# Kernel optimization log

Hardware: AMD Instinct MI355X
Metric: run time of the kernel (lower is better)

Reference implementation:

```python
import jax, jax.numpy as jnp
from jax import lax
import numpy as np

N = 8192
N_ITERS = 10  # ipf(W, 10, 1, 1): row target = 1, col target = 1


def setup_inputs() -> dict:
    key = jax.random.key(0)
    W = jax.random.normal(key, (N, N), dtype=jnp.float32)
    return {"W": W}


def reference(W):
    def step(M, _):
        # row-sum normalize to target 1, then col-sum normalize to target 1
        M = M / jnp.sum(M, axis=1, keepdims=True)
        M = M / jnp.sum(M, axis=0, keepdims=True)
        return M, None

    M = jnp.abs(W)
    M, _ = lax.scan(step, M, None, length=N_ITERS)
    return M
```

## Files before the change

kernel.cpp:

```cpp
#include <hip/hip_runtime.h>

#define N 8192

__device__ __forceinline__ unsigned int f2bf_rne(float f) {
    unsigned int u = __float_as_uint(f);
    u += 0x7fffu + ((u >> 16) & 1u);
    return u >> 16;
}
__device__ __forceinline__ unsigned int pack2(float a, float b) {
    return f2bf_rne(a) | (f2bf_rne(b) << 16);
}
__device__ __forceinline__ float bf_lo(unsigned int u) { return __uint_as_float(u << 16); }
__device__ __forceinline__ float bf_hi(unsigned int u) { return __uint_as_float(u & 0xffff0000u); }

__global__ __launch_bounds__(256) void prep(const float* __restrict__ W,
                                            unsigned int* __restrict__ A,
                                            float* __restrict__ R,
                                            float* __restrict__ b0) {
    const int tid = threadIdx.x;
    if (blockIdx.x < 32) b0[blockIdx.x * 256 + tid] = 0.0f;

    const int wave = tid >> 6, lane = tid & 63;
    const int row = blockIdx.x * 4 + wave;
    const float4* wr = (const float4*)(W + (size_t)row * N);
    uint4* ar = (uint4*)(A + (size_t)row * (N / 2));
    float s = 0.0f;
#pragma unroll 4
    for (int it = 0; it < 16; it++) {
        int g = it * 64 + lane;
        float4 w0 = wr[2 * g];
        float4 w1 = wr[2 * g + 1];
        uint4 p;
        p.x = pack2(fabsf(w0.x), fabsf(w0.y));
        p.y = pack2(fabsf(w0.z), fabsf(w0.w));
        p.z = pack2(fabsf(w1.x), fabsf(w1.y));
        p.w = pack2(fabsf(w1.z), fabsf(w1.w));
        ar[g] = p;
        s += ((bf_lo(p.x) + bf_hi(p.x)) + (bf_lo(p.y) + bf_hi(p.y))) +
             ((bf_lo(p.z) + bf_hi(p.z)) + (bf_lo(p.w) + bf_hi(p.w)));
    }
    for (int off = 32; off > 0; off >>= 1) s += __shfl_down(s, off);
    if (lane == 0) R[row] = 1.0f / s;
}

__global__ __launch_bounds__(256) void pass_rows(const unsigned short* __restrict__ A,
                                                 const float* __restrict__ b_prev,
                                                 float* __restrict__ R,
                                                 float* __restrict__ b_next) {
    __shared__ float crcp[N];
    const int tid = threadIdx.x;
#pragma unroll
    for (int k = 0; k < 8; k++) {
        int f = k * 256 + tid;
        float4 b = ((const float4*)b_prev)[f];
        float4 c;
        c.x = 1.0f / b.x; c.y = 1.0f / b.y; c.z = 1.0f / b.z; c.w = 1.0f / b.w;
        ((float4*)crcp)[f] = c;
    }
    if (tid < 8) b_next[blockIdx.x * 8 + tid] = 0.0f;
    __syncthreads();

    const int wave = tid >> 6, lane = tid & 63;
    for (int rr = 0; rr < 2; rr++) {
        const int row = blockIdx.x * 8 + wave * 2 + rr;
        const uint2* ar = (const uint2*)(A + (size_t)row * N);
        float4 a0 = {0, 0, 0, 0}, a1 = {0, 0, 0, 0};
#pragma unroll 8
        for (int k = 0; k < 32; k += 2) {
            int f0 = k * 64 + lane;
            int f1 = f0 + 64;
            uint2 u0 = ar[f0];
            uint2 u1 = ar[f1];
            float4 c0 = ((const float4*)crcp)[f0];
            float4 c1 = ((const float4*)crcp)[f1];
            a0.x = fmaf(bf_lo(u0.x), c0.x, a0.x);
            a0.y = fmaf(bf_hi(u0.x), c0.y, a0.y);
            a0.z = fmaf(bf_lo(u0.y), c0.z, a0.z);
            a0.w = fmaf(bf_hi(u0.y), c0.w, a0.w);
            a1.x = fmaf(bf_lo(u1.x), c1.x, a1.x);
            a1.y = fmaf(bf_hi(u1.x), c1.y, a1.y);
            a1.z = fmaf(bf_lo(u1.y), c1.z, a1.z);
            a1.w = fmaf(bf_hi(u1.y), c1.w, a1.w);
        }
        float s = ((a0.x + a1.x) + (a0.y + a1.y)) + ((a0.z + a1.z) + (a0.w + a1.w));
        for (int off = 32; off > 0; off >>= 1) s += __shfl_down(s, off);
        if (lane == 0) R[row] = 1.0f / s;
    }
}

__global__ __launch_bounds__(256) void pass_cols(const unsigned short* __restrict__ A,
                                                 const float* __restrict__ R,
                                                 float* __restrict__ b_next) {
    __shared__ float rloc[128];
    const int tid = threadIdx.x;
    const int ctile = blockIdx.x & 7;
    const int chunk = blockIdx.x >> 3;
    const int row0 = chunk * 128;

    if (tid < 128) rloc[tid] = R[row0 + tid];
    __syncthreads();

    const int f = ctile * 256 + tid;
    const uint2* Af = (const uint2*)A;
    float4 acc = {0, 0, 0, 0};
#pragma unroll 4
    for (int i = 0; i < 128; i++) {
        uint2 u = Af[(size_t)(row0 + i) * (N / 4) + f];
        float r = rloc[i];
        acc.x = fmaf(bf_lo(u.x), r, acc.x);
        acc.y = fmaf(bf_hi(u.x), r, acc.y);
        acc.z = fmaf(bf_lo(u.y), r, acc.z);
        acc.w = fmaf(bf_hi(u.y), r, acc.w);
    }
    float* dst = b_next + f * 4;
    atomicAdd(dst + 0, acc.x);
    atomicAdd(dst + 1, acc.y);
    atomicAdd(dst + 2, acc.z);
    atomicAdd(dst + 3, acc.w);
}

__global__ __launch_bounds__(256) void finalize(const float* __restrict__ W,
                                                const float* __restrict__ R,
                                                const float* __restrict__ b_last,
                                                float* __restrict__ out) {
    __shared__ float crcp[N];
    const int tid = threadIdx.x;
#pragma unroll
    for (int k = 0; k < 8; k++) {
        int f = k * 256 + tid;
        float4 b = ((const float4*)b_last)[f];
        float4 c;
        c.x = 1.0f / b.x; c.y = 1.0f / b.y; c.z = 1.0f / b.z; c.w = 1.0f / b.w;
        ((float4*)crcp)[f] = c;
    }
    __syncthreads();

    const int wave = tid >> 6, lane = tid & 63;
    const int row0 = blockIdx.x * 8 + wave * 2;
    for (int rr = 0; rr < 2; rr++) {
        const int row = row0 + rr;
        const float r = R[row];
        const float4* wr = (const float4*)(W + (size_t)row * N);
        float4* orow = (float4*)(out + (size_t)row * N);
#pragma unroll 4
        for (int k = 0; k < 32; k++) {
            int f = k * 64 + lane;
            float4 w = wr[f];
            float4 c = ((const float4*)crcp)[f];
            float4 o;
            o.x = r * fabsf(w.x) * c.x;
            o.y = r * fabsf(w.y) * c.y;
            o.z = r * fabsf(w.z) * c.z;
            o.w = r * fabsf(w.w) * c.w;
            orow[f] = o;
        }
    }
}

extern "C" void kernel_launch(void* const* d_in, const int* in_sizes, int n_in,
                              void* d_out, int out_size, void* d_ws, size_t ws_size,
                              hipStream_t stream) {
    const float* W = (const float*)d_in[0];
    float* out = (float*)d_out;

    unsigned short* A = (unsigned short*)d_out;

    float* R  = (float*)d_ws;
    float* b0 = R + N;
    float* b1 = b0 + N;

    prep<<<2048, 256, 0, stream>>>(W, (unsigned int*)A, R, b0);
    pass_cols<<<512, 256, 0, stream>>>(A, R, b0);

    float* bprev = b0;
    float* bnext = b1;
    for (int k = 2; k <= 10; k++) {
        pass_rows<<<1024, 256, 0, stream>>>(A, bprev, R, bnext);
        pass_cols<<<512, 256, 0, stream>>>(A, R, bnext);
        float* t = bprev; bprev = bnext; bnext = t;
    }
    finalize<<<1024, 256, 0, stream>>>(W, R, bprev, out);
}
```

Measured before the change: 956.2 us.

## Fuse row and column passes into one register-resident pass with partial column sums

Each block loads two rows per wave of the bf16 matrix into registers once, computes the row sums against cached column reciprocals, then accumulates the row-scaled values into shared-memory column sums. It writes per-block partials that a separate kernel reduces and inverts. This removes the second full read of the matrix per iteration and the global atomics. In exchange it adds a partial-sum buffer write/read, LDS atomics and high register pressure.

```diff
diff --git a/kernel.cpp b/kernel.cpp
--- a/kernel.cpp
+++ b/kernel.cpp
@@ -1,6 +1,9 @@
 #include <hip/hip_runtime.h>
 
 #define N 8192
+#define GBLK 512
+#define RPB 16
+#define TPB 512
 
 __device__ __forceinline__ unsigned int f2bf_rne(float f) {
     unsigned int u = __float_as_uint(f);
@@ -15,11 +18,8 @@
 
 __global__ __launch_bounds__(256) void prep(const float* __restrict__ W,
                                             unsigned int* __restrict__ A,
-                                            float* __restrict__ R,
-                                            float* __restrict__ b0) {
-    const int tid = threadIdx.x;
-    if (blockIdx.x < 32) b0[blockIdx.x * 256 + tid] = 0.0f;
-
+                                            float* __restrict__ R) {
+    const int tid = threadIdx.x;
     const int wave = tid >> 6, lane = tid & 63;
     const int row = blockIdx.x * 4 + wave;
     const float4* wr = (const float4*)(W + (size_t)row * N);
@@ -43,95 +43,159 @@
     if (lane == 0) R[row] = 1.0f / s;
 }
 
-__global__ __launch_bounds__(256) void pass_rows(const unsigned short* __restrict__ A,
-                                                 const float* __restrict__ b_prev,
-                                                 float* __restrict__ R,
-                                                 float* __restrict__ b_next) {
+template <int SKIP_ROWS>
+__global__ __launch_bounds__(TPB, 2) void fused_pass(
+    const unsigned short* __restrict__ Au,
+    const float* __restrict__ crcp_g,
+    const float* __restrict__ R_in,
+    float* __restrict__ R_out,
+    float* __restrict__ partial)
+{
     __shared__ float crcp[N];
+    __shared__ float csum[N];
+
+    const int tid = threadIdx.x;
+    const int wave = tid >> 6, lane = tid & 63;
+
+    {
+        float4* dz = (float4*)csum;
+        const float4 z = {0.f, 0.f, 0.f, 0.f};
+#pragma unroll
+        for (int k = 0; k < 4; k++) dz[k * TPB + tid] = z;
+    }
+    if (!SKIP_ROWS) {
+        const float4* src = (const float4*)crcp_g;
+        float4* dc = (float4*)crcp;
+#pragma unroll
+        for (int k = 0; k < 4; k++) {
+            int f = k * TPB + tid;
+            dc[f ^ ((f >> 3) & 1)] = src[f];
+        }
+    }
+    __syncthreads();
+
+    const int rowA = blockIdx.x * RPB + wave * 2;
+    const uint4* pA = (const uint4*)(Au + (size_t)rowA * N);
+    const uint4* pB = (const uint4*)(Au + (size_t)(rowA + 1) * N);
+    uint4 ra[16], rb[16];
+#pragma unroll
+    for (int g = 0; g < 16; g++) ra[g] = pA[g * 64 + lane];
+#pragma unroll
+    for (int g = 0; g < 16; g++) rb[g] = pB[g * 64 + lane];
+
+    float Rva, Rvb;
+    if (SKIP_ROWS) {
+        Rva = R_in[rowA];
+        Rvb = R_in[rowA + 1];
+    } else {
+        const float4* c4 = (const float4*)crcp;
+        const int sw = (lane >> 2) & 1;
+        float4 aA = {0.f, 0.f, 0.f, 0.f}, aB = {0.f, 0.f, 0.f, 0.f};
+#pragma unroll
+        for (int g = 0; g < 16; g++) {
+            const int s0 = g * 128 + 2 * lane;
+            float4 c0 = c4[s0 + sw];
+            float4 c1 = c4[s0 + 1 - sw];
+            aA.x = fmaf(bf_lo(ra[g].x), c0.x, aA.x);
+            aA.y = fmaf(bf_hi(ra[g].x), c0.y, aA.y);
+            aA.z = fmaf(bf_lo(ra[g].y), c0.z, aA.z);
+            aA.w = fmaf(bf_hi(ra[g].y), c0.w, aA.w);
+            aA.x = fmaf(bf_lo(ra[g].z), c1.x, aA.x);
+            aA.y = fmaf(bf_hi(ra[g].z), c1.y, aA.y);
+            aA.z = fmaf(bf_lo(ra[g].w), c1.z, aA.z);
+            aA.w = fmaf(bf_hi(ra[g].w), c1.w, aA.w);
+            aB.x = fmaf(bf_lo(rb[g].x), c0.x, aB.x);
+            aB.y = fmaf(bf_hi(rb[g].x), c0.y, aB.y);
+            aB.z = fmaf(bf_lo(rb[g].y), c0.z, aB.z);
+            aB.w = fmaf(bf_hi(rb[g].y), c0.w, aB.w);
+            aB.x = fmaf(bf_lo(rb[g].z), c1.x, aB.x);
+            aB.y = fmaf(bf_hi(rb[g].z), c1.y, aB.y);
+            aB.z = fmaf(bf_lo(rb[g].w), c1.z, aB.z);
+            aB.w = fmaf(bf_hi(rb[g].w), c1.w, aB.w);
+        }
+        float sA = (aA.x + aA.y) + (aA.z + aA.w);
+        float sB = (aB.x + aB.y) + (aB.z + aB.w);
+#pragma unroll
+        for (int off = 32; off > 0; off >>= 1) {
+            sA += __shfl_xor(sA, off);
+            sB += __shfl_xor(sB, off);
+        }
+        Rva = 1.0f / sA;
+        Rvb = 1.0f / sB;
+        if (lane == 0) {
+            R_out[rowA] = Rva;
+            R_out[rowA + 1] = Rvb;
+        }
+    }
+
+    const int xl = (lane >> 3) & 7;
+#pragma unroll
+    for (int g = 0; g < 16; g++) {
+        const int cb = g * 512 + lane * 8;
+        float v0 = fmaf(bf_lo(ra[g].x), Rva, bf_lo(rb[g].x) * Rvb);
+        float v1 = fmaf(bf_hi(ra[g].x), Rva, bf_hi(rb[g].x) * Rvb);
+        float v2 = fmaf(bf_lo(ra[g].y), Rva, bf_lo(rb[g].y) * Rvb);
+        float v3 = fmaf(bf_hi(ra[g].y), Rva, bf_hi(rb[g].y) * Rvb);
+        float v4 = fmaf(bf_lo(ra[g].z), Rva, bf_lo(rb[g].z) * Rvb);
+        float v5 = fmaf(bf_hi(ra[g].z), Rva, bf_hi(rb[g].z) * Rvb);
+        float v6 = fmaf(bf_lo(ra[g].w), Rva, bf_lo(rb[g].w) * Rvb);
+        float v7 = fmaf(bf_hi(ra[g].w), Rva, bf_hi(rb[g].w) * Rvb);
+        atomicAdd(&csum[cb + (0 ^ xl)], v0);
+        atomicAdd(&csum[cb + (1 ^ xl)], v1);
+        atomicAdd(&csum[cb + (2 ^ xl)], v2);
+        atomicAdd(&csum[cb + (3 ^ xl)], v3);
+        atomicAdd(&csum[cb + (4 ^ xl)], v4);
+        atomicAdd(&csum[cb + (5 ^ xl)], v5);
+        atomicAdd(&csum[cb + (6 ^ xl)], v6);
+        atomicAdd(&csum[cb + (7 ^ xl)], v7);
+    }
+    __syncthreads();
+
+    float4* dst = (float4*)(partial + (size_t)blockIdx.x * N);
+#pragma unroll
+    for (int k = 0; k < 4; k++) {
+        const int f = k * TPB + tid;
+        const int c0 = 4 * f;
+        const int x = (c0 >> 6) & 7;
+        float4 v;
+        v.x = csum[(c0 + 0) ^ x];
+        v.y = csum[(c0 + 1) ^ x];
+        v.z = csum[(c0 + 2) ^ x];
+        v.w = csum[(c0 + 3) ^ x];
+        dst[f] = v;
+    }
+}
+
+__global__ __launch_bounds__(256) void reduce_cols(const float* __restrict__ partial,
+                                                   float* __restrict__ crcp_g) {
+    __shared__ float sh[256];
+    const int tid = threadIdx.x;
+    const int col = blockIdx.x * 32 + (tid & 31);
+    const int grp = tid >> 5;
+    const float* p = partial + (size_t)(grp * 64) * N + col;
+    float s = 0.f;
+#pragma unroll 8
+    for (int k = 0; k < 64; k++) s += p[(size_t)k * N];
+    sh[tid] = s;
+    __syncthreads();
+    if (tid < 32) {
+        float t = sh[tid];
+#pragma unroll
+        for (int g = 1; g < 8; g++) t += sh[g * 32 + tid];
+        crcp_g[col] = 1.0f / t;
+    }
+}
+
+__global__ __launch_bounds__(256) void finalize(const float* __restrict__ W,
+                                                const float* __restrict__ R,
+                                                const float* __restrict__ crcp_g,
+                                                float* __restrict__ out) {
+    __shared__ float crl[N];
     const int tid = threadIdx.x;
 #pragma unroll
     for (int k = 0; k < 8; k++) {
         int f = k * 256 + tid;
-        float4 b = ((const float4*)b_prev)[f];
-        float4 c;
-        c.x = 1.0f / b.x; c.y = 1.0f / b.y; c.z = 1.0f / b.z; c.w = 1.0f / b.w;
-        ((float4*)crcp)[f] = c;
-    }
-    if (tid < 8) b_next[blockIdx.x * 8 + tid] = 0.0f;
-    __syncthreads();
-
-    const int wave = tid >> 6, lane = tid & 63;
-    for (int rr = 0; rr < 2; rr++) {
-        const int row = blockIdx.x * 8 + wave * 2 + rr;
-        const uint2* ar = (const uint2*)(A + (size_t)row * N);
-        float4 a0 = {0, 0, 0, 0}, a1 = {0, 0, 0, 0};
-#pragma unroll 8
-        for (int k = 0; k < 32; k += 2) {
-            int f0 = k * 64 + lane;
-            int f1 = f0 + 64;
-            uint2 u0 = ar[f0];
-            uint2 u1 = ar[f1];
-            float4 c0 = ((const float4*)crcp)[f0];
-            float4 c1 = ((const float4*)crcp)[f1];
-            a0.x = fmaf(bf_lo(u0.x), c0.x, a0.x);
-            a0.y = fmaf(bf_hi(u0.x), c0.y, a0.y);
-            a0.z = fmaf(bf_lo(u0.y), c0.z, a0.z);
-            a0.w = fmaf(bf_hi(u0.y), c0.w, a0.w);
-            a1.x = fmaf(bf_lo(u1.x), c1.x, a1.x);
-            a1.y = fmaf(bf_hi(u1.x), c1.y, a1.y);
-            a1.z = fmaf(bf_lo(u1.y), c1.z, a1.z);
-            a1.w = fmaf(bf_hi(u1.y), c1.w, a1.w);
-        }
-        float s = ((a0.x + a1.x) + (a0.y + a1.y)) + ((a0.z + a1.z) + (a0.w + a1.w));
-        for (int off = 32; off > 0; off >>= 1) s += __shfl_down(s, off);
-        if (lane == 0) R[row] = 1.0f / s;
-    }
-}
-
-__global__ __launch_bounds__(256) void pass_cols(const unsigned short* __restrict__ A,
-                                                 const float* __restrict__ R,
-                                                 float* __restrict__ b_next) {
-    __shared__ float rloc[128];
-    const int tid = threadIdx.x;
-    const int ctile = blockIdx.x & 7;
-    const int chunk = blockIdx.x >> 3;
-    const int row0 = chunk * 128;
-
-    if (tid < 128) rloc[tid] = R[row0 + tid];
-    __syncthreads();
-
-    const int f = ctile * 256 + tid;
-    const uint2* Af = (const uint2*)A;
-    float4 acc = {0, 0, 0, 0};
-#pragma unroll 4
-    for (int i = 0; i < 128; i++) {
-        uint2 u = Af[(size_t)(row0 + i) * (N / 4) + f];
-        float r = rloc[i];
-        acc.x = fmaf(bf_lo(u.x), r, acc.x);
-        acc.y = fmaf(bf_hi(u.x), r, acc.y);
-        acc.z = fmaf(bf_lo(u.y), r, acc.z);
-        acc.w = fmaf(bf_hi(u.y), r, acc.w);
-    }
-    float* dst = b_next + f * 4;
-    atomicAdd(dst + 0, acc.x);
-    atomicAdd(dst + 1, acc.y);
-    atomicAdd(dst + 2, acc.z);
-    atomicAdd(dst + 3, acc.w);
-}
-
-__global__ __launch_bounds__(256) void finalize(const float* __restrict__ W,
-                                                const float* __restrict__ R,
-                                                const float* __restrict__ b_last,
-                                                float* __restrict__ out) {
-    __shared__ float crcp[N];
-    const int tid = threadIdx.x;
-#pragma unroll
-    for (int k = 0; k < 8; k++) {
-        int f = k * 256 + tid;
-        float4 b = ((const float4*)b_last)[f];
-        float4 c;
-        c.x = 1.0f / b.x; c.y = 1.0f / b.y; c.z = 1.0f / b.z; c.w = 1.0f / b.w;
-        ((float4*)crcp)[f] = c;
+        ((float4*)crl)[f] = ((const float4*)crcp_g)[f];
     }
     __syncthreads();
 
@@ -146,7 +210,7 @@
         for (int k = 0; k < 32; k++) {
             int f = k * 64 + lane;
             float4 w = wr[f];
-            float4 c = ((const float4*)crcp)[f];
+            float4 c = ((const float4*)crl)[f];
             float4 o;
             o.x = r * fabsf(w.x) * c.x;
             o.y = r * fabsf(w.y) * c.y;
@@ -165,19 +229,23 @@
 
     unsigned short* A = (unsigned short*)d_out;
 
-    float* R  = (float*)d_ws;
-    float* b0 = R + N;
-    float* b1 = b0 + N;
-
-    prep<<<2048, 256, 0, stream>>>(W, (unsigned int*)A, R, b0);
-    pass_cols<<<512, 256, 0, stream>>>(A, R, b0);
-
-    float* bprev = b0;
-    float* bnext = b1;
+    float* R = (float*)d_ws;
+    float* crcp_g = R + N;
+    float* partial;
+    const size_t vec_bytes = (size_t)2 * N * sizeof(float);
+    const size_t part_bytes = (size_t)GBLK * N * sizeof(float);
+    if (ws_size >= vec_bytes + part_bytes)
+        partial = crcp_g + N;
+    else
+        partial = (float*)((char*)d_out + (size_t)N * N * 2);
+
+    prep<<<2048, 256, 0, stream>>>(W, (unsigned int*)A, R);
+    fused_pass<1><<<GBLK, TPB, 0, stream>>>(A, crcp_g, R, R, partial);
+    reduce_cols<<<256, 256, 0, stream>>>(partial, crcp_g);
+
     for (int k = 2; k <= 10; k++) {
-        pass_rows<<<1024, 256, 0, stream>>>(A, bprev, R, bnext);
-        pass_cols<<<512, 256, 0, stream>>>(A, R, bnext);
-        float* t = bprev; bprev = bnext; bnext = t;
-    }
-    finalize<<<1024, 256, 0, stream>>>(W, R, bprev, out);
-}
+        fused_pass<0><<<GBLK, TPB, 0, stream>>>(A, crcp_g, R, R, partial);
+        reduce_cols<<<256, 256, 0, stream>>>(partial, crcp_g);
+    }
+    finalize<<<1024, 256, 0, stream>>>(W, R, crcp_g, out);
+}
```

After: 2.783 ms. 191% more time.
